# Kernel tuning notes

Measured on AMD Instinct MI355X. Metric: run time of the kernel, lower is better.

Reference implementation:

```python
import jax, jax.numpy as jnp
import numpy as np

RADIUS = 0.1
LOOP = False


def _radius_adj(pos, r, loop):
    # pairwise squared distances via GEMM: ||a-b||^2 = ||a||^2 + ||b||^2 - 2 a.b
    sq = jnp.sum(pos * pos, axis=-1)                      # [N]
    d2 = sq[:, None] + sq[None, :] - 2.0 * (pos @ pos.T)  # [N, N]
    adj = d2 <= r * r
    if not loop:
        n = pos.shape[0]
        adj = adj & ~jnp.eye(n, dtype=bool)
    return adj


def setup_inputs() -> dict:
    key = jax.random.key(0)
    k1, _ = jax.random.split(key)
    N = 8192
    domain = jnp.ones((3,), dtype=jnp.float32)
    positions = jax.random.uniform(k1, (N, 3), dtype=jnp.float32) * domain
    return {"positions": positions, "domain": domain}


def reference(positions, domain):
    # Pass 1: unshifted radius graph.
    adj = _radius_adj(positions, RADIUS, LOOP)
    # Passes 2-4: shift by factor*domain, wrap back into the box, re-run
    # radius graph; torch.unique dedup of concatenated edge lists is exactly
    # the boolean OR of adjacencies.
    for factor in (0.25, 0.5, 0.75):
        shifted = jnp.remainder(positions + factor * domain, domain)
        adj = adj | _radius_adj(shifted, RADIUS, LOOP)
    return adj  # [N, N] bool adjacency == deduped edge_index
```

## Files before the change

kernel.cpp:

```cpp
#include <hip/hip_runtime.h>
#include <math.h>


__global__ __launch_bounds__(256) void gg_shift_kernel(
    const float* __restrict__ pos, const float* __restrict__ dom,
    float4* __restrict__ sp, int n)
{
#pragma clang fp contract(off)
    int i = blockIdx.x * blockDim.x + threadIdx.x;
    if (i >= n) return;
    float x = pos[3 * i + 0];
    float y = pos[3 * i + 1];
    float z = pos[3 * i + 2];
    float dx = dom[0], dy = dom[1], dz = dom[2];
#pragma unroll
    for (int k = 0; k < 4; ++k) {
        float sx, sy, sz;
        if (k == 0) {
            sx = x; sy = y; sz = z;
        } else {
            float f = 0.25f * (float)k;
            sx = fmodf(x + f * dx, dx);
            sy = fmodf(y + f * dy, dy);
            sz = fmodf(z + f * dz, dz);
        }
        float sq = ((sx * sx) + (sy * sy)) + (sz * sz);
        sp[(size_t)i * 4 + k] = make_float4(sx, sy, sz, sq);
    }
}

__global__ __launch_bounds__(256) void gg_adj_kernel(
    const float4* __restrict__ sp, const float* __restrict__ dom,
    int* __restrict__ out, int n)
{
    const int tid = threadIdx.x;
    const int tj = tid & 63;
    const int ti = tid >> 6;
    const int jbase = blockIdx.x * 256 + tj * 4;
    const int ibase = blockIdx.y * 32;

    const float dom0 = dom[0], dom1 = dom[1], dom2 = dom[2];

    __shared__ float4 si[32][4];
    for (int t = tid; t < 128; t += 256)
        si[t >> 2][t & 3] = sp[(size_t)(ibase + (t >> 2)) * 4 + (t & 3)];

    float4 jd0[4];
#pragma unroll
    for (int p = 0; p < 4; ++p)
        jd0[p] = sp[(size_t)(jbase + p) * 4 + 0];

    __syncthreads();

    const float RR = 0.01f;
    const float LO = 0.01f - 3e-5f;
    const float HI = 0.01f + 3e-5f;

    for (int iter = 0; iter < 8; ++iter) {
        const int irow = iter * 4 + ti;
        const int i = ibase + irow;
        const float4 i0 = si[irow][0];

        int4 res;
        int* r = &res.x;
#pragma unroll
        for (int p = 0; p < 4; ++p) {
            const float ax = fabsf(i0.x - jd0[p].x);
            const float ay = fabsf(i0.y - jd0[p].y);
            const float az = fabsf(i0.z - jd0[p].z);
            const float mx = fminf(ax, dom0 - ax);
            const float my = fminf(ay, dom1 - ay);
            const float mz = fminf(az, dom2 - az);
            const float d2m = mx * mx + my * my + mz * mz;
            bool b = d2m <= RR;
            if (__builtin_expect(d2m >= LO && d2m <= HI, 0)) {
#pragma clang fp contract(off)
                b = false;
#pragma unroll 1
                for (int k = 0; k < 4; ++k) {
                    const float4 iv = si[irow][k];
                    const float4 jv = sp[(size_t)(jbase + p) * 4 + k];
                    float dot = __builtin_fmaf(iv.z, jv.z,
                                __builtin_fmaf(iv.y, jv.y, iv.x * jv.x));
                    float d2 = (iv.w + jv.w) - (2.0f * dot);
                    if (d2 <= RR) b = true;
                }
            }
            r[p] = (b && (i != jbase + p)) ? 1 : 0;
        }
        *reinterpret_cast<int4*>(&out[(size_t)i * n + jbase]) = res;
    }
}

extern "C" void kernel_launch(void* const* d_in, const int* in_sizes, int n_in,
                              void* d_out, int out_size, void* d_ws, size_t ws_size,
                              hipStream_t stream) {
    const float* pos = (const float*)d_in[0];
    const float* dom = (const float*)d_in[1];
    const int n = in_sizes[0] / 3;

    float4* sp = (float4*)d_ws;
    int* out = (int*)d_out;

    gg_shift_kernel<<<(n + 255) / 256, 256, 0, stream>>>(pos, dom, sp, n);

    dim3 grid(n / 256, n / 32);
    gg_adj_kernel<<<grid, 256, 0, stream>>>(sp, dom, out, n);
}
```

Measured before the change: 51.05 us.

## Restructure adjacency kernel to one block per output row reading raw positions

Replaces the 2D-tiled adjacency kernel with a kernel that launches one block per row i. Each thread loops over eight passes of four j columns, loading j coordinates directly from the packed xyz array with three float4 loads instead of strided float4 shift records. This removes the shared-memory staging and __syncthreads, and makes each block write one contiguous 32 KB output row. In exchange the grid grows to 8192 blocks, the i point is read per block without reuse across rows, and the rare exact fallback path reads both i and j records from global memory.

```diff
diff --git a/kernel.cpp b/kernel.cpp
--- a/kernel.cpp
+++ b/kernel.cpp
@@ -29,45 +29,43 @@
     }
 }
 
-__global__ __launch_bounds__(256) void gg_adj_kernel(
-    const float4* __restrict__ sp, const float* __restrict__ dom,
-    int* __restrict__ out, int n)
+__global__ __launch_bounds__(256) void gg_adj_row_kernel(
+    const float* __restrict__ pos, const float4* __restrict__ sp,
+    const float* __restrict__ dom, int* __restrict__ out, int n)
 {
+    const int y = blockIdx.x;
     const int tid = threadIdx.x;
-    const int tj = tid & 63;
-    const int ti = tid >> 6;
-    const int jbase = blockIdx.x * 256 + tj * 4;
-    const int ibase = blockIdx.y * 32;
 
+    const float ix = pos[3 * y + 0];
+    const float iy = pos[3 * y + 1];
+    const float iz = pos[3 * y + 2];
     const float dom0 = dom[0], dom1 = dom[1], dom2 = dom[2];
 
-    __shared__ float4 si[32][4];
-    for (int t = tid; t < 128; t += 256)
-        si[t >> 2][t & 3] = sp[(size_t)(ibase + (t >> 2)) * 4 + (t & 3)];
+    const float RR  = 0.01f;
+    const float LO  = 0.01f - 3e-5f;
+    const float HI  = 0.01f + 3e-5f;
 
-    float4 jd0[4];
-#pragma unroll
-    for (int p = 0; p < 4; ++p)
-        jd0[p] = sp[(size_t)(jbase + p) * 4 + 0];
+    int* orow = &out[(size_t)y * n];
 
-    __syncthreads();
+    for (int pass = 0; pass < 8; ++pass) {
+        const int jbase = pass * 1024 + tid * 4;
 
-    const float RR = 0.01f;
-    const float LO = 0.01f - 3e-5f;
-    const float HI = 0.01f + 3e-5f;
-
-    for (int iter = 0; iter < 8; ++iter) {
-        const int irow = iter * 4 + ti;
-        const int i = ibase + irow;
-        const float4 i0 = si[irow][0];
+        const float4 j0 = *(const float4*)&pos[3 * jbase + 0];
+        const float4 j1 = *(const float4*)&pos[3 * jbase + 4];
+        const float4 j2 = *(const float4*)&pos[3 * jbase + 8];
+        float jx[4], jy[4], jz[4];
+        jx[0] = j0.x; jy[0] = j0.y; jz[0] = j0.z;
+        jx[1] = j0.w; jy[1] = j1.x; jz[1] = j1.y;
+        jx[2] = j1.z; jy[2] = j1.w; jz[2] = j2.x;
+        jx[3] = j2.y; jy[3] = j2.z; jz[3] = j2.w;
 
         int4 res;
         int* r = &res.x;
 #pragma unroll
         for (int p = 0; p < 4; ++p) {
-            const float ax = fabsf(i0.x - jd0[p].x);
-            const float ay = fabsf(i0.y - jd0[p].y);
-            const float az = fabsf(i0.z - jd0[p].z);
+            const float ax = fabsf(ix - jx[p]);
+            const float ay = fabsf(iy - jy[p]);
+            const float az = fabsf(iz - jz[p]);
             const float mx = fminf(ax, dom0 - ax);
             const float my = fminf(ay, dom1 - ay);
             const float mz = fminf(az, dom2 - az);
@@ -78,7 +76,7 @@
                 b = false;
 #pragma unroll 1
                 for (int k = 0; k < 4; ++k) {
-                    const float4 iv = si[irow][k];
+                    const float4 iv = sp[(size_t)y * 4 + k];
                     const float4 jv = sp[(size_t)(jbase + p) * 4 + k];
                     float dot = __builtin_fmaf(iv.z, jv.z,
                                 __builtin_fmaf(iv.y, jv.y, iv.x * jv.x));
@@ -86,9 +84,9 @@
                     if (d2 <= RR) b = true;
                 }
             }
-            r[p] = (b && (i != jbase + p)) ? 1 : 0;
+            r[p] = (b && (y != jbase + p)) ? 1 : 0;
         }
-        *reinterpret_cast<int4*>(&out[(size_t)i * n + jbase]) = res;
+        *reinterpret_cast<int4*>(&orow[jbase]) = res;
     }
 }
 
@@ -104,6 +102,5 @@
 
     gg_shift_kernel<<<(n + 255) / 256, 256, 0, stream>>>(pos, dom, sp, n);
 
-    dim3 grid(n / 256, n / 32);
-    gg_adj_kernel<<<grid, 256, 0, stream>>>(sp, dom, out, n);
+    gg_adj_row_kernel<<<n, 256, 0, stream>>>(pos, sp, dom, out, n);
 }
```

New measurement: 52.85 us. +3.5%, slower.
